# Kernel tuning notes

Hardware: AMD Instinct MI355X
Metric: run time of the kernel (lower is better)

## Reference

```python
import jax, jax.numpy as jnp
import numpy as np

HIDDEN = 2048
NUM_HEADS = 16
HEAD_DIM = HIDDEN // NUM_HEADS


def setup_inputs() -> dict:
    key = jax.random.key(0)
    ks = jax.random.split(key, 10)
    B, S = 2, 2048
    scale = 1.0 / np.sqrt(HIDDEN)
    inp = {
        "x": jax.random.normal(ks[0], (B, S, HIDDEN), dtype=jnp.float32),
        "attention_mask": jnp.zeros((B, S), dtype=jnp.float32),
        "Wq": jax.random.normal(ks[1], (HIDDEN, HIDDEN), dtype=jnp.float32) * scale,
        "bq": jnp.zeros((HIDDEN,), dtype=jnp.float32),
        "Wk": jax.random.normal(ks[2], (HIDDEN, HIDDEN), dtype=jnp.float32) * scale,
        "bk": jnp.zeros((HIDDEN,), dtype=jnp.float32),
        "Wv": jax.random.normal(ks[3], (HIDDEN, HIDDEN), dtype=jnp.float32) * scale,
        "bv": jnp.zeros((HIDDEN,), dtype=jnp.float32),
        "Wo": jax.random.normal(ks[4], (HIDDEN, HIDDEN), dtype=jnp.float32) * scale,
        "bo": jnp.zeros((HIDDEN,), dtype=jnp.float32),
    }
    return inp


def _split_heads(t):
    # [B, S, H*D] -> [B, H, S, D]
    B, S, _ = t.shape
    return t.reshape(B, S, NUM_HEADS, HEAD_DIM).transpose(0, 2, 1, 3)


def reference(x, attention_mask, Wq, bq, Wk, bk, Wv, bv, Wo, bo):
    B, S, _ = x.shape
    # Linear layers: y = x @ W^T + b (torch nn.Linear convention)
    q = _split_heads(x @ Wq.T + bq)  # [B, H, S, D]
    k = _split_heads(x @ Wk.T + bk)
    v = _split_heads(x @ Wv.T + bv)
    scale = 1.0 / jnp.sqrt(jnp.asarray(HEAD_DIM, dtype=x.dtype))
    scores = jnp.einsum("bhqd,bhkd->bhqk", q, k) * scale  # [B, H, S, S]
    scores = scores + attention_mask[:, None, None, :]  # additive mask broadcast
    attn = jax.nn.softmax(scores, axis=-1)
    out = jnp.einsum("bhqk,bhkd->bhqd", attn, v)  # [B, H, S, D]
    out = out.transpose(0, 2, 1, 3).reshape(B, S, HIDDEN)
    return out @ Wo.T + bo
```

## Files before the change

kernel.cpp:

```cpp
#include <hip/hip_runtime.h>
#include <math.h>

constexpr int S_LEN = 2048;
constexpr int HID   = 2048;
constexpr int NH    = 16;
constexpr int HD    = 128;

typedef __attribute__((ext_vector_type(8))) short short8;
typedef __attribute__((ext_vector_type(4))) float floatx4;

static __device__ __forceinline__ ushort f2bf(float f) {
  union { float f; unsigned u; } v; v.f = f;
  unsigned r = (v.u + 0x7fffu + ((v.u >> 16) & 1u)) >> 16;
  return (ushort)r;
}
static __device__ __forceinline__ ushort f2bf_fast(float f) {
  union { float f; unsigned u; } v; v.f = f;
  return (ushort)((v.u + 0x8000u) >> 16);
}

static __device__ __forceinline__ void glds16(const ushort* g, ushort* l) {
  __builtin_amdgcn_global_load_lds(
      (const __attribute__((address_space(1))) void*)g,
      (__attribute__((address_space(3))) void*)l, 16, 0, 0);
}

static __device__ __forceinline__ void cvt4(ushort* dst, const float* src, size_t i) {
  const float4 v = ((const float4*)src)[i];
  ushort4 u = {f2bf(v.x), f2bf(v.y), f2bf(v.z), f2bf(v.w)};
  ((ushort4*)dst)[i] = u;
}

__global__ __launch_bounds__(256)
void convert_all(const float* __restrict__ x,
                 const float* __restrict__ wq, const float* __restrict__ wk,
                 const float* __restrict__ wv, const float* __restrict__ wo,
                 ushort* __restrict__ xb, ushort* __restrict__ wqb,
                 ushort* __restrict__ wkb, ushort* __restrict__ wvb,
                 ushort* __restrict__ wob) {
  const size_t gid = blockIdx.x * 256 + threadIdx.x;
  const size_t T = gridDim.x * 256;
  const size_t NX = (size_t)4096 * HID / 4;
  const size_t NW = (size_t)HID * HID / 4;
  for (size_t i = gid; i < NX; i += T) cvt4(xb, x, i);
  for (size_t i = gid; i < NW; i += T) {
    cvt4(wqb, wq, i);
    cvt4(wkb, wk, i);
    cvt4(wvb, wv, i);
    cvt4(wob, wo, i);
  }
}

template <bool BF16OUT>
__device__ __forceinline__
void gemm_core(const ushort* __restrict__ A, const ushort* __restrict__ W,
               const float* __restrict__ bias, void* __restrict__ Cv,
               int m0, int n0) {
  __shared__ __align__(16) ushort As[4096];
  __shared__ __align__(16) ushort Bs[4096];

  const int tid  = threadIdx.x;
  const int lane = tid & 63;
  const int w    = tid >> 6;
  const int wm   = w >> 1, wn = w & 1;
  const int n16  = lane & 15, q4 = lane >> 4;

  const int sr = lane >> 2;
  const int sc = (lane & 3) ^ ((lane >> 4) & 3);
  const ushort* ag0 = A + (size_t)(m0 + w*32 + sr) * HID + sc*8;
  const ushort* ag1 = ag0 + (size_t)16 * HID;
  const ushort* bg0 = W + (size_t)(n0 + w*32 + sr) * HID + sc*8;
  const ushort* bg1 = bg0 + (size_t)16 * HID;
  ushort* al0 = As + (w*2 + 0) * 512;
  ushort* al1 = As + (w*2 + 1) * 512;
  ushort* bl0 = Bs + (w*2 + 0) * 512;
  ushort* bl1 = Bs + (w*2 + 1) * 512;

  const int fp = n16*4 + (q4 ^ ((n16 >> 2) & 3));

  floatx4 acc[4][4];
  #pragma unroll
  for (int i = 0; i < 4; ++i)
    #pragma unroll
    for (int j = 0; j < 4; ++j) acc[i][j] = (floatx4)0.f;

  for (int kb0 = 0; kb0 < HID; kb0 += 32) {
    __syncthreads();
    glds16(ag0 + kb0, al0);
    glds16(ag1 + kb0, al1);
    glds16(bg0 + kb0, bl0);
    glds16(bg1 + kb0, bl1);
    __syncthreads();

    short8 af[4], bf[4];
    #pragma unroll
    for (int t = 0; t < 4; ++t) {
      af[t] = *(const short8*)&As[(wm*4 + t)*512 + fp*8];
      bf[t] = *(const short8*)&Bs[(wn*4 + t)*512 + fp*8];
    }
    #pragma unroll
    for (int mt = 0; mt < 4; ++mt)
      #pragma unroll
      for (int nt = 0; nt < 4; ++nt)
        acc[mt][nt] = __builtin_amdgcn_mfma_f32_16x16x32_bf16(af[mt], bf[nt], acc[mt][nt], 0, 0, 0);
  }

  float bv4[4];
  #pragma unroll
  for (int nt = 0; nt < 4; ++nt) bv4[nt] = bias[n0 + wn*64 + nt*16 + n16];
  #pragma unroll
  for (int mt = 0; mt < 4; ++mt)
    #pragma unroll
    for (int nt = 0; nt < 4; ++nt)
      #pragma unroll
      for (int r = 0; r < 4; ++r) {
        const int row = m0 + wm*64 + mt*16 + q4*4 + r;
        const int col = n0 + wn*64 + nt*16 + n16;
        if (BF16OUT)
          ((ushort*)Cv)[(size_t)row * HID + col] = f2bf(acc[mt][nt][r] + bv4[nt]);
        else
          ((float*)Cv)[(size_t)row * HID + col] = acc[mt][nt][r] + bv4[nt];
      }
}

__global__ __launch_bounds__(256)
void gemm_qkv(const ushort* __restrict__ xb,
              const ushort* __restrict__ wqb, const ushort* __restrict__ wkb,
              const ushort* __restrict__ wvb,
              const float* __restrict__ bq, const float* __restrict__ bk,
              const float* __restrict__ bv,
              ushort* __restrict__ qb, ushort* __restrict__ kb_, ushort* __restrict__ vb) {
  const ushort* W; const float* bias; ushort* C;
  if (blockIdx.z == 0)      { W = wqb; bias = bq; C = qb;  }
  else if (blockIdx.z == 1) { W = wkb; bias = bk; C = kb_; }
  else                      { W = wvb; bias = bv; C = vb;  }
  gemm_core<true>(xb, W, bias, C, blockIdx.y * 128, blockIdx.x * 128);
}

__global__ __launch_bounds__(256)
void gemm_o(const ushort* __restrict__ ao, const ushort* __restrict__ wob,
            const float* __restrict__ bo, float* __restrict__ out) {
  gemm_core<false>(ao, wob, bo, out, blockIdx.y * 128, blockIdx.x * 128);
}

__global__ __launch_bounds__(256)
void transpose_v(const ushort* __restrict__ vb, ushort* __restrict__ vt) {
  __shared__ ushort T[64][72];
  const int t  = threadIdx.x;
  const int bh = blockIdx.z;
  const int b = bh >> 4, h = bh & 15;
  const int s0 = blockIdx.x * 64;
  const int d0 = blockIdx.y * 64;
  {
    const int r = t >> 2, c = (t & 3) * 16;
    const ushort* src = vb + (size_t)(b*S_LEN + s0 + r)*HID + h*HD + d0 + c;
    *(uint4*)&T[r][c]     = *(const uint4*)src;
    *(uint4*)&T[r][c + 8] = *(const uint4*)(src + 8);
  }
  __syncthreads();
  {
    const int dd = t >> 2, c = (t & 3) * 16;
    ushort tmp[16];
    #pragma unroll
    for (int j = 0; j < 16; ++j) tmp[j] = T[c + j][dd];
    ushort* dst = vt + (size_t)((b*NH + h)*HD + d0 + dd)*S_LEN + s0 + c;
    *(uint4*)dst       = *(uint4*)tmp;
    *(uint4*)(dst + 8) = *(uint4*)(tmp + 8);
  }
}

__global__ __launch_bounds__(512)
void attn_mfma(const ushort* __restrict__ qb, const ushort* __restrict__ kbuf,
               const ushort* __restrict__ vtb, const float* __restrict__ mask,
               ushort* __restrict__ ao) {
  __shared__ __align__(16) ushort Ks[64 * 136];
  __shared__ __align__(16) ushort Vs[128 * 72];
  __shared__ __align__(16) ushort Ps[8 * 16 * 72];

  const int tid  = threadIdx.x;
  const int w    = tid >> 6;
  const int lane = tid & 63;
  const int n16  = lane & 15;
  const int q4   = lane >> 4;
  const int b  = blockIdx.y >> 4;
  const int h  = blockIdx.y & 15;
  const int q0 = blockIdx.x * 128;
  const float scale = 0.08838834764831845f;

  ushort* Pw = Ps + w * (16 * 72);

  short8 aq[4];
  {
    const ushort* qrow = qb + (size_t)(b*S_LEN + q0 + w*16 + n16)*HID + h*HD;
    #pragma unroll
    for (int kc = 0; kc < 4; ++kc)
      aq[kc] = *(const short8*)(qrow + kc*32 + q4*8);
  }

  floatx4 oacc[8];
  float lp[4];
  #pragma unroll
  for (int dt = 0; dt < 8; ++dt) oacc[dt] = (floatx4)0.f;
  #pragma unroll
  for (int r = 0; r < 4; ++r) lp[r] = 0.f;

  const int krow = tid >> 4, kc16 = tid & 15;
  const int vrow = tid >> 3, vc8  = tid & 7;
  const ushort* kg = kbuf + (size_t)(b*S_LEN + krow)*HID + h*HD + kc16*8;
  const ushort* vg = vtb + ((size_t)(b*NH + h)*HD + vrow)*S_LEN + vc8*8;
  const size_t k32 = (size_t)32 * HID;
  const size_t v64 = (size_t)64 * S_LEN;

  uint4 kr0 = *(const uint4*)(kg);
  uint4 kr1 = *(const uint4*)(kg + k32);
  uint4 vr0 = *(const uint4*)(vg);
  uint4 vr1 = *(const uint4*)(vg + v64);

  for (int kb0 = 0; kb0 < S_LEN; kb0 += 64) {
    __syncthreads();
    *(uint4*)&Ks[krow*136 + kc16*8]        = kr0;
    *(uint4*)&Ks[(krow + 32)*136 + kc16*8] = kr1;
    *(uint4*)&Vs[vrow*72 + vc8*8]          = vr0;
    *(uint4*)&Vs[(vrow + 64)*72 + vc8*8]   = vr1;
    if (kb0 + 64 < S_LEN) {
      const size_t ko = (size_t)(kb0 + 64) * HID;
      kr0 = *(const uint4*)(kg + ko);
      kr1 = *(const uint4*)(kg + ko + k32);
      vr0 = *(const uint4*)(vg + kb0 + 64);
      vr1 = *(const uint4*)(vg + kb0 + 64 + v64);
    }
    __syncthreads();

    floatx4 acc[4];
    #pragma unroll
    for (int nt = 0; nt < 4; ++nt) acc[nt] = (floatx4)0.f;
    #pragma unroll
    for (int nt = 0; nt < 4; ++nt) {
      #pragma unroll
      for (int kc = 0; kc < 4; ++kc) {
        const short8 bk = *(const short8*)&Ks[(nt*16 + n16)*136 + kc*32 + q4*8];
        acc[nt] = __builtin_amdgcn_mfma_f32_16x16x32_bf16(aq[kc], bk, acc[nt], 0, 0, 0);
      }
    }

    float mk[4];
    #pragma unroll
    for (int nt = 0; nt < 4; ++nt)
      mk[nt] = mask[(size_t)b*S_LEN + kb0 + nt*16 + n16];

    #pragma unroll
    for (int r = 0; r < 4; ++r) {
      float p[4];
      #pragma unroll
      for (int nt = 0; nt < 4; ++nt) p[nt] = __expf(acc[nt][r] * scale + mk[nt]);
      lp[r] += (p[0] + p[1]) + (p[2] + p[3]);
      #pragma unroll
      for (int nt = 0; nt < 4; ++nt)
        Pw[(q4*4 + r)*72 + nt*16 + n16] = f2bf_fast(p[nt]);
    }

    #pragma unroll
    for (int kc2 = 0; kc2 < 2; ++kc2) {
      const short8 ap = *(const short8*)&Pw[n16*72 + kc2*32 + q4*8];
      #pragma unroll
      for (int dt = 0; dt < 8; ++dt) {
        const short8 bvf = *(const short8*)&Vs[(dt*16 + n16)*72 + kc2*32 + q4*8];
        oacc[dt] = __builtin_amdgcn_mfma_f32_16x16x32_bf16(ap, bvf, oacc[dt], 0, 0, 0);
      }
    }
  }

  #pragma unroll
  for (int r = 0; r < 4; ++r) {
    float l = lp[r];
    l += __shfl_xor(l, 1);
    l += __shfl_xor(l, 2);
    l += __shfl_xor(l, 4);
    l += __shfl_xor(l, 8);
    lp[r] = 1.0f / l;
  }

  #pragma unroll
  for (int r = 0; r < 4; ++r) {
    const size_t rowoff = (size_t)(b*S_LEN + q0 + w*16 + q4*4 + r)*HID + h*HD;
    #pragma unroll
    for (int dt = 0; dt < 8; ++dt)
      ao[rowoff + dt*16 + n16] = f2bf(oacc[dt][r] * lp[r]);
  }
}

extern "C" void kernel_launch(void* const* d_in, const int* in_sizes, int n_in,
                              void* d_out, int out_size, void* d_ws, size_t ws_size,
                              hipStream_t stream) {
  (void)n_in; (void)out_size; (void)ws_size;
  const float* x    = (const float*)d_in[0];
  const float* mask = (const float*)d_in[1];
  const float* Wq   = (const float*)d_in[2];
  const float* bq   = (const float*)d_in[3];
  const float* Wk   = (const float*)d_in[4];
  const float* bk   = (const float*)d_in[5];
  const float* Wv   = (const float*)d_in[6];
  const float* bv   = (const float*)d_in[7];
  const float* Wo   = (const float*)d_in[8];
  const float* bo   = (const float*)d_in[9];
  float* out = (float*)d_out;

  const int B = in_sizes[0] / (S_LEN * HID);
  const int M = B * S_LEN;
  const size_t MH = (size_t)M * HID;
  const size_t WW = (size_t)HID * HID;

  ushort* xb   = (ushort*)d_ws;
  ushort* wqb  = xb   + MH;
  ushort* wkb  = wqb  + WW;
  ushort* wvb  = wkb  + WW;
  ushort* wob  = wvb  + WW;
  ushort* qb   = wob  + WW;
  ushort* kbuf = qb   + MH;
  ushort* vb   = kbuf + MH;
  ushort* vt   = vb   + MH;
  ushort* ao   = vb;

  convert_all<<<512, 256, 0, stream>>>(x, Wq, Wk, Wv, Wo, xb, wqb, wkb, wvb, wob);
  gemm_qkv<<<dim3(HID/128, M/128, 3), 256, 0, stream>>>(xb, wqb, wkb, wvb, bq, bk, bv, qb, kbuf, vb);
  transpose_v<<<dim3(S_LEN/64, HD/64, B*NH), 256, 0, stream>>>(vb, vt);
  attn_mfma<<<dim3(S_LEN/128, B*NH), 512, 0, stream>>>(qb, kbuf, vt, mask, ao);
  gemm_o<<<dim3(HID/128, M/128), 256, 0, stream>>>(ao, wob, bo, out);
}
```

Baseline: 420.4 us.

## Fuse V transpose into attention staging and give each wave 32 query rows

```diff
diff --git a/kernel.cpp b/kernel.cpp
--- a/kernel.cpp
+++ b/kernel.cpp
@@ -143,39 +143,13 @@
   gemm_core<false>(ao, wob, bo, out, blockIdx.y * 128, blockIdx.x * 128);
 }
 
-__global__ __launch_bounds__(256)
-void transpose_v(const ushort* __restrict__ vb, ushort* __restrict__ vt) {
-  __shared__ ushort T[64][72];
-  const int t  = threadIdx.x;
-  const int bh = blockIdx.z;
-  const int b = bh >> 4, h = bh & 15;
-  const int s0 = blockIdx.x * 64;
-  const int d0 = blockIdx.y * 64;
-  {
-    const int r = t >> 2, c = (t & 3) * 16;
-    const ushort* src = vb + (size_t)(b*S_LEN + s0 + r)*HID + h*HD + d0 + c;
-    *(uint4*)&T[r][c]     = *(const uint4*)src;
-    *(uint4*)&T[r][c + 8] = *(const uint4*)(src + 8);
-  }
-  __syncthreads();
-  {
-    const int dd = t >> 2, c = (t & 3) * 16;
-    ushort tmp[16];
-    #pragma unroll
-    for (int j = 0; j < 16; ++j) tmp[j] = T[c + j][dd];
-    ushort* dst = vt + (size_t)((b*NH + h)*HD + d0 + dd)*S_LEN + s0 + c;
-    *(uint4*)dst       = *(uint4*)tmp;
-    *(uint4*)(dst + 8) = *(uint4*)(tmp + 8);
-  }
-}
-
-__global__ __launch_bounds__(512)
+__global__ __launch_bounds__(256, 2)
 void attn_mfma(const ushort* __restrict__ qb, const ushort* __restrict__ kbuf,
-               const ushort* __restrict__ vtb, const float* __restrict__ mask,
+               const ushort* __restrict__ vb, const float* __restrict__ mask,
                ushort* __restrict__ ao) {
   __shared__ __align__(16) ushort Ks[64 * 136];
   __shared__ __align__(16) ushort Vs[128 * 72];
-  __shared__ __align__(16) ushort Ps[8 * 16 * 72];
+  __shared__ __align__(16) ushort Ps[4 * 32 * 72];
 
   const int tid  = threadIdx.x;
   const int w    = tid >> 6;
@@ -187,59 +161,73 @@
   const int q0 = blockIdx.x * 128;
   const float scale = 0.08838834764831845f;
 
-  ushort* Pw = Ps + w * (16 * 72);
-
-  short8 aq[4];
-  {
-    const ushort* qrow = qb + (size_t)(b*S_LEN + q0 + w*16 + n16)*HID + h*HD;
+  ushort* Pw = Ps + w * (32 * 72);
+
+  short8 aq[2][4];
+  #pragma unroll
+  for (int mt = 0; mt < 2; ++mt) {
+    const ushort* qrow = qb + (size_t)(b*S_LEN + q0 + w*32 + mt*16 + n16)*HID + h*HD;
     #pragma unroll
     for (int kc = 0; kc < 4; ++kc)
-      aq[kc] = *(const short8*)(qrow + kc*32 + q4*8);
-  }
-
-  floatx4 oacc[8];
-  float lp[4];
-  #pragma unroll
-  for (int dt = 0; dt < 8; ++dt) oacc[dt] = (floatx4)0.f;
-  #pragma unroll
-  for (int r = 0; r < 4; ++r) lp[r] = 0.f;
-
-  const int krow = tid >> 4, kc16 = tid & 15;
-  const int vrow = tid >> 3, vc8  = tid & 7;
-  const ushort* kg = kbuf + (size_t)(b*S_LEN + krow)*HID + h*HD + kc16*8;
-  const ushort* vg = vtb + ((size_t)(b*NH + h)*HD + vrow)*S_LEN + vc8*8;
-  const size_t k32 = (size_t)32 * HID;
-  const size_t v64 = (size_t)64 * S_LEN;
-
-  uint4 kr0 = *(const uint4*)(kg);
-  uint4 kr1 = *(const uint4*)(kg + k32);
-  uint4 vr0 = *(const uint4*)(vg);
-  uint4 vr1 = *(const uint4*)(vg + v64);
+      aq[mt][kc] = *(const short8*)(qrow + kc*32 + q4*8);
+  }
+
+  floatx4 oacc[2][8];
+  float lp[2][4];
+  #pragma unroll
+  for (int mt = 0; mt < 2; ++mt) {
+    #pragma unroll
+    for (int dt = 0; dt < 8; ++dt) oacc[mt][dt] = (floatx4)0.f;
+    #pragma unroll
+    for (int r = 0; r < 4; ++r) lp[mt][r] = 0.f;
+  }
+
+  const int srow = tid >> 2;
+  const int sseg = (tid & 3) * 32;
+  const ushort* kg = kbuf + (size_t)(b*S_LEN + srow)*HID + h*HD + sseg;
+  const ushort* vg = vb   + (size_t)(b*S_LEN + srow)*HID + h*HD + sseg;
+
+  uint4 kr[4], vr[4];
+  #pragma unroll
+  for (int j = 0; j < 4; ++j) {
+    kr[j] = *(const uint4*)(kg + j*8);
+    vr[j] = *(const uint4*)(vg + j*8);
+  }
 
   for (int kb0 = 0; kb0 < S_LEN; kb0 += 64) {
     __syncthreads();
-    *(uint4*)&Ks[krow*136 + kc16*8]        = kr0;
-    *(uint4*)&Ks[(krow + 32)*136 + kc16*8] = kr1;
-    *(uint4*)&Vs[vrow*72 + vc8*8]          = vr0;
-    *(uint4*)&Vs[(vrow + 64)*72 + vc8*8]   = vr1;
+    #pragma unroll
+    for (int j = 0; j < 4; ++j)
+      *(uint4*)&Ks[srow*136 + sseg + j*8] = kr[j];
+    const ushort* vsc = (const ushort*)vr;
+    #pragma unroll
+    for (int j = 0; j < 32; ++j)
+      Vs[(sseg + j)*72 + srow] = vsc[j];
     if (kb0 + 64 < S_LEN) {
-      const size_t ko = (size_t)(kb0 + 64) * HID;
-      kr0 = *(const uint4*)(kg + ko);
-      kr1 = *(const uint4*)(kg + ko + k32);
-      vr0 = *(const uint4*)(vg + kb0 + 64);
-      vr1 = *(const uint4*)(vg + kb0 + 64 + v64);
+      const size_t ko = (size_t)64 * HID;
+      const ushort* kg2 = kg + (size_t)(kb0 + 64) * HID;
+      const ushort* vg2 = vg + (size_t)(kb0 + 64) * HID;
+      #pragma unroll
+      for (int j = 0; j < 4; ++j) {
+        kr[j] = *(const uint4*)(kg2 + j*8);
+        vr[j] = *(const uint4*)(vg2 + j*8);
+      }
+      (void)ko;
     }
     __syncthreads();
 
-    floatx4 acc[4];
-    #pragma unroll
-    for (int nt = 0; nt < 4; ++nt) acc[nt] = (floatx4)0.f;
+    floatx4 acc[2][4];
+    #pragma unroll
+    for (int mt = 0; mt < 2; ++mt)
+      #pragma unroll
+      for (int nt = 0; nt < 4; ++nt) acc[mt][nt] = (floatx4)0.f;
     #pragma unroll
     for (int nt = 0; nt < 4; ++nt) {
       #pragma unroll
       for (int kc = 0; kc < 4; ++kc) {
         const short8 bk = *(const short8*)&Ks[(nt*16 + n16)*136 + kc*32 + q4*8];
-        acc[nt] = __builtin_amdgcn_mfma_f32_16x16x32_bf16(aq[kc], bk, acc[nt], 0, 0, 0);
+        acc[0][nt] = __builtin_amdgcn_mfma_f32_16x16x32_bf16(aq[0][kc], bk, acc[0][nt], 0, 0, 0);
+        acc[1][nt] = __builtin_amdgcn_mfma_f32_16x16x32_bf16(aq[1][kc], bk, acc[1][nt], 0, 0, 0);
       }
     }
 
@@ -249,44 +237,52 @@
       mk[nt] = mask[(size_t)b*S_LEN + kb0 + nt*16 + n16];
 
     #pragma unroll
-    for (int r = 0; r < 4; ++r) {
-      float p[4];
-      #pragma unroll
-      for (int nt = 0; nt < 4; ++nt) p[nt] = __expf(acc[nt][r] * scale + mk[nt]);
-      lp[r] += (p[0] + p[1]) + (p[2] + p[3]);
-      #pragma unroll
-      for (int nt = 0; nt < 4; ++nt)
-        Pw[(q4*4 + r)*72 + nt*16 + n16] = f2bf_fast(p[nt]);
-    }
+    for (int mt = 0; mt < 2; ++mt)
+      #pragma unroll
+      for (int r = 0; r < 4; ++r) {
+        float p[4];
+        #pragma unroll
+        for (int nt = 0; nt < 4; ++nt) p[nt] = __expf(acc[mt][nt][r] * scale + mk[nt]);
+        lp[mt][r] += (p[0] + p[1]) + (p[2] + p[3]);
+        #pragma unroll
+        for (int nt = 0; nt < 4; ++nt)
+          Pw[(mt*16 + q4*4 + r)*72 + nt*16 + n16] = f2bf_fast(p[nt]);
+      }
 
     #pragma unroll
     for (int kc2 = 0; kc2 < 2; ++kc2) {
-      const short8 ap = *(const short8*)&Pw[n16*72 + kc2*32 + q4*8];
+      const short8 ap0 = *(const short8*)&Pw[(0*16 + n16)*72 + kc2*32 + q4*8];
+      const short8 ap1 = *(const short8*)&Pw[(1*16 + n16)*72 + kc2*32 + q4*8];
       #pragma unroll
       for (int dt = 0; dt < 8; ++dt) {
         const short8 bvf = *(const short8*)&Vs[(dt*16 + n16)*72 + kc2*32 + q4*8];
-        oacc[dt] = __builtin_amdgcn_mfma_f32_16x16x32_bf16(ap, bvf, oacc[dt], 0, 0, 0);
-      }
-    }
-  }
-
-  #pragma unroll
-  for (int r = 0; r < 4; ++r) {
-    float l = lp[r];
-    l += __shfl_xor(l, 1);
-    l += __shfl_xor(l, 2);
-    l += __shfl_xor(l, 4);
-    l += __shfl_xor(l, 8);
-    lp[r] = 1.0f / l;
-  }
-
-  #pragma unroll
-  for (int r = 0; r < 4; ++r) {
-    const size_t rowoff = (size_t)(b*S_LEN + q0 + w*16 + q4*4 + r)*HID + h*HD;
-    #pragma unroll
-    for (int dt = 0; dt < 8; ++dt)
-      ao[rowoff + dt*16 + n16] = f2bf(oacc[dt][r] * lp[r]);
-  }
+        oacc[0][dt] = __builtin_amdgcn_mfma_f32_16x16x32_bf16(ap0, bvf, oacc[0][dt], 0, 0, 0);
+        oacc[1][dt] = __builtin_amdgcn_mfma_f32_16x16x32_bf16(ap1, bvf, oacc[1][dt], 0, 0, 0);
+      }
+    }
+  }
+
+  #pragma unroll
+  for (int mt = 0; mt < 2; ++mt)
+    #pragma unroll
+    for (int r = 0; r < 4; ++r) {
+      float l = lp[mt][r];
+      l += __shfl_xor(l, 1);
+      l += __shfl_xor(l, 2);
+      l += __shfl_xor(l, 4);
+      l += __shfl_xor(l, 8);
+      lp[mt][r] = 1.0f / l;
+    }
+
+  #pragma unroll
+  for (int mt = 0; mt < 2; ++mt)
+    #pragma unroll
+    for (int r = 0; r < 4; ++r) {
+      const size_t rowoff = (size_t)(b*S_LEN + q0 + w*32 + mt*16 + q4*4 + r)*HID + h*HD;
+      #pragma unroll
+      for (int dt = 0; dt < 8; ++dt)
+        ao[rowoff + dt*16 + n16] = f2bf(oacc[mt][dt][r] * lp[mt][r]);
+    }
 }
 
 extern "C" void kernel_launch(void* const* d_in, const int* in_sizes, int n_in,
@@ -318,12 +314,10 @@
   ushort* qb   = wob  + WW;
   ushort* kbuf = qb   + MH;
   ushort* vb   = kbuf + MH;
-  ushort* vt   = vb   + MH;
-  ushort* ao   = vb;
+  ushort* ao   = xb;
 
   convert_all<<<512, 256, 0, stream>>>(x, Wq, Wk, Wv, Wo, xb, wqb, wkb, wvb, wob);
   gemm_qkv<<<dim3(HID/128, M/128, 3), 256, 0, stream>>>(xb, wqb, wkb, wvb, bq, bk, bv, qb, kbuf, vb);
-  transpose_v<<<dim3(S_LEN/64, HD/64, B*NH), 256, 0, stream>>>(vb, vt);
-  attn_mfma<<<dim3(S_LEN/128, B*NH), 512, 0, stream>>>(qb, kbuf, vt, mask, ao);
+  attn_mfma<<<dim3(S_LEN/128, B*NH), 256, 0, stream>>>(qb, kbuf, vb, mask, ao);
   gemm_o<<<dim3(HID/128, M/128), 256, 0, stream>>>(ao, wob, bo, out);
 }
```

Result: slower. 443.7 us (+5.5%).
